# Performance work log

Hardware: AMD Instinct MI355X
Metric: run time of the kernel (lower is better)

Reference implementation:

```python
import jax, jax.numpy as jnp
import numpy as np

B, S, H = 2, 512, 1024
D = 24            # hdim_proj_dim
MLP_H = 96        # hdim_mlp_hidden
VAL_IN = 2 * H    # concat_only
OUT_HID = 2 * max(128, H // 2)  # 1024


def setup_inputs() -> dict:
    key = jax.random.key(0)
    ks = jax.random.split(key, 12)
    sc = 0.02
    return {
        "H_j": jax.random.normal(ks[0], (B, S, H), jnp.float32),
        "H_i": jax.random.normal(ks[1], (B, S, H), jnp.float32),
        "attn_mask": jnp.ones((B, S), jnp.float32),
        "p_j": jax.random.normal(ks[2], (H, D), jnp.float32) * sc,
        "p_i": jax.random.normal(ks[3], (H, D), jnp.float32) * sc,
        "W1": jax.random.normal(ks[4], (4 * D, MLP_H), jnp.float32) * sc,
        "b1": jnp.zeros((MLP_H,), jnp.float32),
        "W2": jax.random.normal(ks[5], (MLP_H, 1), jnp.float32) * sc,
        "b2": jnp.zeros((1,), jnp.float32),
        "Wv1": jax.random.normal(ks[6], (VAL_IN, OUT_HID), jnp.float32) * sc,
        "bv1": jnp.zeros((OUT_HID,), jnp.float32),
        "Wv2": jax.random.normal(ks[7], (OUT_HID, H), jnp.float32) * sc,
        "bv2": jnp.zeros((H,), jnp.float32),
        "alpha": jnp.asarray(0.05, jnp.float32),
    }


def reference(H_j, H_i, attn_mask, p_j, p_i, W1, b1, W2, b2, Wv1, bv1, Wv2, bv2, alpha):
    # Low-dim projections: [B,S,D]
    Zj = jnp.einsum('bsh,hd->bsd', H_j, p_j)
    Zi = jnp.einsum('bsh,hd->bsd', H_i, p_i)
    # 4-term pairwise features: [B,S,S,4D]
    Zj_b = jnp.broadcast_to(Zj[:, :, None, :], (B, S, S, D))
    Zi_b = jnp.broadcast_to(Zi[:, None, :, :], (B, S, S, D))
    pair = jnp.concatenate([Zj_b, Zi_b, Zj_b * Zi_b, jnp.abs(Zj_b - Zi_b)], axis=-1)
    # Pair-score MLP -> logits [B,S,S]
    h = jax.nn.relu(jnp.einsum('bjif,fm->bjim', pair, W1) + b1)
    logits = (jnp.einsum('bjim,mo->bjio', h, W2) + b2)[..., 0]
    # additive key-side mask (same as torch _expand_mask_last)
    logits = logits + (1.0 - attn_mask)[:, None, :] * jnp.finfo(logits.dtype).min
    # token_temp == 1.0 -> no scaling
    probs = jax.nn.softmax(logits, axis=-1)  # over keys i
    ctx = jnp.einsum('bji,bih->bjh', probs, H_i)  # [B,S,H]
    # Value fusion MLP (concat_only), dropout is identity in eval
    msg_in = jnp.concatenate([ctx, H_j], axis=-1)  # [B,S,2H]
    msg = jax.nn.relu(jnp.einsum('bsf,fo->bso', msg_in, Wv1) + bv1)
    msg = jnp.einsum('bso,oh->bsh', msg, Wv2) + bv2
    return alpha * msg
```

## Files before the change

### kernel.cpp

```cpp
#include <hip/hip_runtime.h>
#include <math.h>

#define B_    2
#define S_    512
#define HDIM  1024
#define D_    24
#define M_    96
#define ROWS  (B_*S_)

typedef _Float16 half8 __attribute__((ext_vector_type(8)));
typedef float    f32x4 __attribute__((ext_vector_type(4)));

__device__ __forceinline__ void transpose_tile(
    const float* __restrict__ in, _Float16* __restrict__ out,
    int R, int C, int xt, int yt, float (*tile)[33], int t) {
  int bx = xt * 32, by = yt * 32;
  int tx = t & 31, ty = t >> 5;
#pragma unroll
  for (int k = 0; k < 4; ++k)
    tile[ty + k * 8][tx] = in[(size_t)(by + ty + k * 8) * C + bx + tx];
  __syncthreads();
#pragma unroll
  for (int k = 0; k < 4; ++k)
    out[(size_t)(bx + ty + k * 8) * R + by + tx] = (_Float16)tile[tx][ty + k * 8];
}

__global__ __launch_bounds__(256) void prep_kernel(
    const float* __restrict__ Hj, const float* __restrict__ Hi,
    const float* __restrict__ pj, const float* __restrict__ pi,
    const float* __restrict__ W1, const float* __restrict__ Wv1,
    const float* __restrict__ Wv2,
    _Float16* __restrict__ HjH, _Float16* __restrict__ HiT,
    _Float16* __restrict__ Wv1T, _Float16* __restrict__ Wv2T,
    _Float16* __restrict__ Wimg, float* __restrict__ Zj,
    float* __restrict__ Zi) {
  __shared__ float tile[32][33];
  const int bid = blockIdx.x;
  const int t = threadIdx.x;

  if (bid < 4) {
    int c = bid * 256 + t;
    half8 v = {};
    if (c < 864) {
      int kc = c / 96, m = c - kc * 96;
#pragma unroll
      for (int e = 0; e < 8; ++e)
        v[e] = (_Float16)W1[(24 + kc * 8 + e) * M_ + m];
    }
    *(half8*)(Wimg + (size_t)c * 8) = v;
  } else if (bid < 1028) {
    int i = (bid - 4) * 256 + t;
    float4 v = ((const float4*)Hj)[i];
    _Float16 o[4] = {(_Float16)v.x, (_Float16)v.y, (_Float16)v.z, (_Float16)v.w};
    ((ushort4*)HjH)[i] = *(ushort4*)o;
  } else if (bid < 2052) {
    int id = bid - 1028;
    int z = id >> 9, rem = id & 511;
    transpose_tile(Hi + (size_t)z * S_ * HDIM, HiT + (size_t)z * HDIM * S_,
                   S_, HDIM, rem & 31, rem >> 5, tile, t);
  } else if (bid < 4100) {
    int id = bid - 2052;
    transpose_tile(Wv1, Wv1T, 2 * HDIM, HDIM, id & 31, id >> 5, tile, t);
  } else if (bid < 5124) {
    int id = bid - 4100;
    transpose_tile(Wv2, Wv2T, HDIM, HDIM, id & 31, id >> 5, tile, t);
  } else {
    int r = (bid - 5124) * 4 + (t >> 6);
    int lane = t & 63;
    float4 a4 = ((const float4*)(Hj + (size_t)r * HDIM))[lane];
    float4 c4 = ((const float4*)(Hi + (size_t)r * HDIM))[lane];
    float accj[D_], acci[D_];
#pragma unroll
    for (int d = 0; d < D_; ++d) { accj[d] = 0.f; acci[d] = 0.f; }
    const float* aa = (const float*)&a4;
    const float* cc = (const float*)&c4;
#pragma unroll
    for (int kk = 0; kk < 4; ++kk) {
      const float4* pj4 = (const float4*)(pj + (size_t)(lane * 4 + kk) * D_);
      const float4* pi4 = (const float4*)(pi + (size_t)(lane * 4 + kk) * D_);
      float a = aa[kk], c = cc[kk];
#pragma unroll
      for (int q = 0; q < 6; ++q) {
        float4 wj = pj4[q], wi = pi4[q];
        accj[q * 4 + 0] = fmaf(a, wj.x, accj[q * 4 + 0]);
        accj[q * 4 + 1] = fmaf(a, wj.y, accj[q * 4 + 1]);
        accj[q * 4 + 2] = fmaf(a, wj.z, accj[q * 4 + 2]);
        accj[q * 4 + 3] = fmaf(a, wj.w, accj[q * 4 + 3]);
        acci[q * 4 + 0] = fmaf(c, wi.x, acci[q * 4 + 0]);
        acci[q * 4 + 1] = fmaf(c, wi.y, acci[q * 4 + 1]);
        acci[q * 4 + 2] = fmaf(c, wi.z, acci[q * 4 + 2]);
        acci[q * 4 + 3] = fmaf(c, wi.w, acci[q * 4 + 3]);
      }
    }
#pragma unroll
    for (int d = 0; d < D_; ++d) {
      for (int off = 32; off > 0; off >>= 1) {
        accj[d] += __shfl_down(accj[d], off, 64);
        acci[d] += __shfl_down(acci[d], off, 64);
      }
    }
    if (lane == 0) {
#pragma unroll
      for (int d = 0; d < D_; ++d) {
        Zj[r * D_ + d] = accj[d];
        Zi[r * D_ + d] = acci[d];
      }
    }
  }
}

#define FOFFB   0
#define WOFFB   40960
#define ZOFFB   (WOFFB + 960*16)
#define LOGOFFB (WOFFB + 16384)
#define ZJOFFB  (LOGOFFB + 2048)
#define W2OFFB  (ZJOFFB + 96)
#define REDOFFB (W2OFFB + 384)
#define LDSB    (REDOFFB + 32)

__global__ __launch_bounds__(256) void pair_fused_kernel(
    const float* __restrict__ Zj, const float* __restrict__ Zi,
    const float* __restrict__ W1, const float* __restrict__ b1,
    const float* __restrict__ W2, const _Float16* __restrict__ Wimg,
    const float* __restrict__ mask, _Float16* __restrict__ probs) {
  __shared__ __attribute__((aligned(16))) char smem[LDSB];
  const int t = threadIdx.x;
  const int w = t >> 6, l = t & 63;
  const int lo = l & 15, hi = l >> 4;
  const int rj = blockIdx.x;
  const int b = rj >> 9;

#pragma unroll
  for (int r = 0; r < 4; ++r) {
    const _Float16* src = Wimg + (size_t)(r * 256 + w * 64 + l) * 8;
    __builtin_amdgcn_global_load_lds(
        (const __attribute__((address_space(1))) void*)src,
        (__attribute__((address_space(3))) void*)(smem + WOFFB + (r * 256 + w * 64) * 16),
        16, 0, 0);
  }
  float* zjL    = (float*)(smem + ZJOFFB);
  float* W2s    = (float*)(smem + W2OFFB);
  float* logits = (float*)(smem + LOGOFFB);
  float* red    = (float*)(smem + REDOFFB);
  if (t < D_) zjL[t] = Zj[(size_t)rj * D_ + t];
  if (t < M_) W2s[t] = W2[t];
  float aj = 0.f;
  if (t < M_) {
    aj = b1[t];
#pragma unroll
    for (int d = 0; d < D_; ++d)
      aj = fmaf(Zj[(size_t)rj * D_ + d], W1[d * M_ + t], aj);
  }
  __syncthreads();
  if (t < M_) {
    half8 v = {};
    v[0] = (_Float16)aj;
    *(half8*)(smem + WOFFB + (864 + t) * 16) = v;
  }

  half8 wf[6][3];
  float w2r[6][4];

  for (int p = 0; p < 2; ++p) {
    {
      int i = p * 256 + t;
      const float* zi = Zi + (size_t)(b * S_ + i) * D_;
      float ziv[D_];
#pragma unroll
      for (int q = 0; q < 6; ++q) {
        float4 v = ((const float4*)zi)[q];
        ziv[q * 4 + 0] = v.x; ziv[q * 4 + 1] = v.y;
        ziv[q * 4 + 2] = v.z; ziv[q * 4 + 3] = v.w;
      }
#pragma unroll
      for (int kc = 0; kc < 3; ++kc) {
        half8 v;
#pragma unroll
        for (int e = 0; e < 8; ++e) v[e] = (_Float16)ziv[kc * 8 + e];
        *(half8*)(smem + FOFFB + (kc * 256 + t) * 16) = v;
      }
#pragma unroll
      for (int kc = 0; kc < 3; ++kc) {
        half8 v;
#pragma unroll
        for (int e = 0; e < 8; ++e) {
          int d = kc * 8 + e;
          v[e] = (_Float16)(zjL[d] * ziv[d]);
        }
        *(half8*)(smem + FOFFB + ((kc + 3) * 256 + t) * 16) = v;
      }
#pragma unroll
      for (int kc = 0; kc < 3; ++kc) {
        half8 v;
#pragma unroll
        for (int e = 0; e < 8; ++e) {
          int d = kc * 8 + e;
          v[e] = (_Float16)fabsf(zjL[d] - ziv[d]);
        }
        *(half8*)(smem + FOFFB + ((kc + 6) * 256 + t) * 16) = v;
      }
      if (p == 0) {
        half8 v = {};
        v[0] = (_Float16)1.0f;
        *(half8*)(smem + FOFFB + (9 * 256 + t) * 16) = v;
      }
    }
    __syncthreads();

    if (p == 0) {
#pragma unroll
      for (int mh = 0; mh < 6; ++mh) {
#pragma unroll
        for (int ks = 0; ks < 3; ++ks) {
          int kc = ks * 4 + hi;
          int off = (kc < 10) ? (WOFFB + (kc * 96 + mh * 16 + lo) * 16) : ZOFFB;
          wf[mh][ks] = *(const half8*)(smem + off);
        }
#pragma unroll
        for (int r = 0; r < 4; ++r) w2r[mh][r] = W2s[mh * 16 + hi * 4 + r];
      }
    }

#pragma unroll
    for (int nt = 0; nt < 4; ++nt) {
      half8 ff[3];
#pragma unroll
      for (int ks = 0; ks < 3; ++ks) {
        int kc = ks * 4 + hi;
        int off = (kc < 10) ? (FOFFB + (kc * 256 + w * 64 + nt * 16 + lo) * 16) : ZOFFB;
        ff[ks] = *(const half8*)(smem + off);
      }
      f32x4 a6[6] = {};
#pragma unroll
      for (int ks = 0; ks < 3; ++ks)
#pragma unroll
        for (int mh = 0; mh < 6; ++mh)
          a6[mh] = __builtin_amdgcn_mfma_f32_16x16x32_f16(wf[mh][ks], ff[ks], a6[mh], 0, 0, 0);
      float part = 0.f;
#pragma unroll
      for (int mh = 0; mh < 6; ++mh)
#pragma unroll
        for (int r = 0; r < 4; ++r)
          part = fmaf(fmaxf(a6[mh][r], 0.f), w2r[mh][r], part);
      part += __shfl_xor(part, 16);
      part += __shfl_xor(part, 32);
      if (hi == 0) logits[p * 256 + w * 64 + nt * 16 + lo] = part;
    }
    __syncthreads();
  }

  float m1 = mask[b * S_ + t], m2 = mask[b * S_ + t + 256];
  float lg1 = logits[t]       + (1.0f - m1) * (-3.40282347e38f);
  float lg2 = logits[t + 256] + (1.0f - m2) * (-3.40282347e38f);
  float mx = fmaxf(lg1, lg2);
#pragma unroll
  for (int off = 32; off > 0; off >>= 1) mx = fmaxf(mx, __shfl_xor(mx, off));
  if (l == 0) red[w] = mx;
  __syncthreads();
  float rmax = fmaxf(fmaxf(red[0], red[1]), fmaxf(red[2], red[3]));
  float e1 = __expf(lg1 - rmax);
  float e2 = __expf(lg2 - rmax);
  float s = e1 + e2;
#pragma unroll
  for (int off = 32; off > 0; off >>= 1) s += __shfl_xor(s, off);
  if (l == 0) red[4 + w] = s;
  __syncthreads();
  float inv = 1.0f / (red[4] + red[5] + red[6] + red[7]);
  probs[(size_t)rj * S_ + t]       = (_Float16)(e1 * inv);
  probs[(size_t)rj * S_ + t + 256] = (_Float16)(e2 * inv);
}

template <bool HASA1, bool RELU, bool FINAL, bool OUTH>
__global__ __launch_bounds__(512) void mfma_gemm_kernel(
    const _Float16* __restrict__ A0, const _Float16* __restrict__ A1,
    const _Float16* __restrict__ Bt, const float* __restrict__ bias,
    const float* __restrict__ alpha_ptr, void* __restrict__ Cout,
    int M, int N, int K0, int K1,
    long aB0, long aB1, long bB, long cB) {
  __shared__ __attribute__((aligned(16))) char smem[65536];
  const int t = threadIdx.x;
  const int w = t >> 6, l = t & 63;
  const int g = w >> 2, wq = w & 3;
  const int K = K0 + K1;
  const int KH = K >> 1;
  const int NT = KH >> 5;
  const int n0 = blockIdx.x * 64, m0 = blockIdx.y * 64;
  const int zb = blockIdx.z;
  const _Float16* A0b = A0 + (size_t)zb * aB0;
  const _Float16* A1b = HASA1 ? (A1 + (size_t)zb * aB1) : nullptr;
  const _Float16* Btb = Bt + (size_t)zb * bB;
  char* gls = smem + (g << 15);

  const int sr = (wq << 4) + (l >> 2);
  const int sk = ((l & 3) ^ ((l >> 3) & 3)) << 3;

  const int mq = wq >> 1, nq = wq & 1;
  int offA[2], offB[2];
#pragma unroll
  for (int i = 0; i < 2; ++i) {
    int ra = mq * 32 + i * 16 + (l & 15);
    offA[i] = ra * 64 + (((l >> 4) ^ ((ra >> 1) & 3)) << 4);
    int rb = nq * 32 + i * 16 + (l & 15);
    offB[i] = 4096 + rb * 64 + (((l >> 4) ^ ((rb >> 1) & 3)) << 4);
  }

  f32x4 acc[2][2] = {};

  auto stage = [&](int tt) {
    char* buf = gls + (tt & 3) * 8192;
    int kg = g * KH + (tt << 5) + sk;
    const _Float16* ga;
    if (HASA1 && kg >= K0) ga = A1b + (size_t)(m0 + sr) * K1 + (kg - K0);
    else                   ga = A0b + (size_t)(m0 + sr) * K0 + kg;
    __builtin_amdgcn_global_load_lds(
        (const __attribute__((address_space(1))) void*)ga,
        (__attribute__((address_space(3))) void*)(buf + (wq << 10)), 16, 0, 0);
    const _Float16* gb = Btb + (size_t)(n0 + sr) * K + kg;
    __builtin_amdgcn_global_load_lds(
        (const __attribute__((address_space(1))) void*)gb,
        (__attribute__((address_space(3))) void*)(buf + 4096 + (wq << 10)), 16, 0, 0);
  };

  stage(0);
  stage(1);
  stage(2);

  for (int tt = 0; tt < NT; ++tt) {
    if (tt + 2 < NT)      asm volatile("s_waitcnt vmcnt(4)" ::: "memory");
    else if (tt + 1 < NT) asm volatile("s_waitcnt vmcnt(2)" ::: "memory");
    else                  asm volatile("s_waitcnt vmcnt(0)" ::: "memory");
    __builtin_amdgcn_s_barrier();
    __builtin_amdgcn_sched_barrier(0);
    const char* buf = gls + (tt & 3) * 8192;
    half8 a0 = *(const half8*)(buf + offA[0]);
    half8 a1 = *(const half8*)(buf + offA[1]);
    half8 b0 = *(const half8*)(buf + offB[0]);
    half8 b1v = *(const half8*)(buf + offB[1]);
    acc[0][0] = __builtin_amdgcn_mfma_f32_16x16x32_f16(a0, b0, acc[0][0], 0, 0, 0);
    acc[0][1] = __builtin_amdgcn_mfma_f32_16x16x32_f16(a0, b1v, acc[0][1], 0, 0, 0);
    acc[1][0] = __builtin_amdgcn_mfma_f32_16x16x32_f16(a1, b0, acc[1][0], 0, 0, 0);
    acc[1][1] = __builtin_amdgcn_mfma_f32_16x16x32_f16(a1, b1v, acc[1][1], 0, 0, 0);
    if (tt + 3 < NT) stage(tt + 3);
  }

  const int lr = l & 15, lq = l >> 4;
  float* redm = (float*)smem;
  __syncthreads();
  if (g == 1) {
#pragma unroll
    for (int mi = 0; mi < 2; ++mi)
#pragma unroll
      for (int ni = 0; ni < 2; ++ni)
#pragma unroll
        for (int rg = 0; rg < 4; ++rg)
          redm[(mq * 32 + mi * 16 + lq * 4 + rg) * 68 + nq * 32 + ni * 16 + lr] =
              acc[mi][ni][rg];
  }
  __syncthreads();
  if (g == 0) {
    const float alpha = FINAL ? *alpha_ptr : 1.0f;
    const size_t cbase = (size_t)zb * cB;
#pragma unroll
    for (int mi = 0; mi < 2; ++mi)
#pragma unroll
      for (int ni = 0; ni < 2; ++ni) {
        int col = n0 + nq * 32 + ni * 16 + lr;
        float bv = bias ? bias[col] : 0.0f;
#pragma unroll
        for (int rg = 0; rg < 4; ++rg) {
          int row = m0 + mq * 32 + mi * 16 + lq * 4 + rg;
          float x = acc[mi][ni][rg] +
                    redm[(mq * 32 + mi * 16 + lq * 4 + rg) * 68 + nq * 32 + ni * 16 + lr] +
                    bv;
          if (RELU) x = fmaxf(x, 0.f);
          if (FINAL) x *= alpha;
          if (OUTH)
            ((_Float16*)Cout)[cbase + (size_t)row * N + col] = (_Float16)x;
          else
            ((float*)Cout)[cbase + (size_t)row * N + col] = x;
        }
      }
  }
}

extern "C" void kernel_launch(void* const* d_in, const int* in_sizes, int n_in,
                              void* d_out, int out_size, void* d_ws, size_t ws_size,
                              hipStream_t stream) {
  const float* Hj   = (const float*)d_in[0];
  const float* Hi   = (const float*)d_in[1];
  const float* mask = (const float*)d_in[2];
  const float* pj   = (const float*)d_in[3];
  const float* pi   = (const float*)d_in[4];
  const float* W1   = (const float*)d_in[5];
  const float* b1   = (const float*)d_in[6];
  const float* W2   = (const float*)d_in[7];
  const float* Wv1  = (const float*)d_in[9];
  const float* bv1  = (const float*)d_in[10];
  const float* Wv2  = (const float*)d_in[11];
  const float* bv2  = (const float*)d_in[12];
  const float* alpha = (const float*)d_in[13];

  char* w = (char*)d_ws;
  float* Zj  = (float*)w;            w += (size_t)ROWS * D_ * 4;
  float* Zi  = (float*)w;            w += (size_t)ROWS * D_ * 4;
  _Float16* Wimg   = (_Float16*)w;   w += (size_t)1024 * 16;
  _Float16* probsH = (_Float16*)w;   w += (size_t)B_ * S_ * S_ * 2;
  _Float16* HjH    = (_Float16*)w;   w += (size_t)ROWS * HDIM * 2;
  _Float16* HiT    = (_Float16*)w;   w += (size_t)B_ * HDIM * S_ * 2;
  _Float16* Wv1T   = (_Float16*)w;   w += (size_t)HDIM * 2 * HDIM * 2;
  _Float16* Wv2T   = (_Float16*)w;   w += (size_t)HDIM * HDIM * 2;
  _Float16* ctxH   = (_Float16*)w;   w += (size_t)ROWS * HDIM * 2;
  _Float16* hidH   = (_Float16*)w;   w += (size_t)ROWS * HDIM * 2;
  float* out = (float*)d_out;

  prep_kernel<<<5380, 256, 0, stream>>>(Hj, Hi, pj, pi, W1, Wv1, Wv2,
                                        HjH, HiT, Wv1T, Wv2T, Wimg, Zj, Zi);

  pair_fused_kernel<<<ROWS, 256, 0, stream>>>(Zj, Zi, W1, b1, W2, Wimg,
                                              mask, probsH);

  mfma_gemm_kernel<false, false, false, true><<<dim3(16, 8, 2), 512, 0, stream>>>(
      probsH, nullptr, HiT, nullptr, nullptr, ctxH,
      S_, HDIM, S_, 0, (long)S_ * S_, 0, (long)HDIM * S_, (long)S_ * HDIM);
  mfma_gemm_kernel<true, true, false, true><<<dim3(16, 16, 1), 512, 0, stream>>>(
      ctxH, HjH, Wv1T, bv1, nullptr, hidH,
      ROWS, HDIM, HDIM, HDIM, 0, 0, 0, 0);
  mfma_gemm_kernel<false, false, true, false><<<dim3(16, 16, 1), 512, 0, stream>>>(
      hidH, nullptr, Wv2T, bv2, alpha, out,
      ROWS, HDIM, HDIM, 0, 0, 0, 0, 0);
}
```

Baseline: 76.22 us.

## Use 64x64 transpose tiles, fuse projections into cast, 4-way split-K GEMM

The prep kernel moves to 64x64 transpose tiles that convert to fp16 in LDS and write 16-byte vectors. The Zj/Zi projections are folded into per-row blocks that also do the Hj fp16 cast, which cuts the prep grid. The GEMM kernel goes from 2-way to 4-way split-K inside 1024-thread blocks with 128KB LDS, and the three partial results are reduced through LDS. s_setprio is also placed around the MFMA sections. The larger LDS and thread count may reduce occupancy, and the shorter per-group K loop gives less pipelining depth.

```diff
diff --git a/kernel.cpp b/kernel.cpp
--- a/kernel.cpp
+++ b/kernel.cpp
@@ -10,19 +10,68 @@
 
 typedef _Float16 half8 __attribute__((ext_vector_type(8)));
 typedef float    f32x4 __attribute__((ext_vector_type(4)));
-
-__device__ __forceinline__ void transpose_tile(
+typedef unsigned short ushort8 __attribute__((ext_vector_type(8)));
+
+__device__ __forceinline__ void transpose_tile64(
     const float* __restrict__ in, _Float16* __restrict__ out,
-    int R, int C, int xt, int yt, float (*tile)[33], int t) {
-  int bx = xt * 32, by = yt * 32;
-  int tx = t & 31, ty = t >> 5;
-#pragma unroll
-  for (int k = 0; k < 4; ++k)
-    tile[ty + k * 8][tx] = in[(size_t)(by + ty + k * 8) * C + bx + tx];
-  __syncthreads();
-#pragma unroll
-  for (int k = 0; k < 4; ++k)
-    out[(size_t)(bx + ty + k * 8) * R + by + tx] = (_Float16)tile[tx][ty + k * 8];
+    int R, int C, int xt, int yt, _Float16* tileh, int t) {
+  int R0 = yt * 64, C0 = xt * 64;
+  {
+    int r = t >> 4, c4 = (t & 15) * 4;
+#pragma unroll
+    for (int i = 0; i < 4; ++i) {
+      float4 v = *(const float4*)(in + (size_t)(R0 + r + i * 16) * C + C0 + c4);
+      _Float16 o[4] = {(_Float16)v.x, (_Float16)v.y, (_Float16)v.z, (_Float16)v.w};
+      *(ushort4*)(tileh + (r + i * 16) * 72 + c4) = *(ushort4*)o;
+    }
+  }
+  __syncthreads();
+  {
+    int r0 = (t & 7) * 8;
+#pragma unroll
+    for (int p = 0; p < 2; ++p) {
+      int c = p * 32 + (t >> 3);
+      _Float16 o[8];
+#pragma unroll
+      for (int e = 0; e < 8; ++e) o[e] = tileh[(r0 + e) * 72 + c];
+      *(ushort8*)(out + (size_t)(C0 + c) * R + R0 + r0) = *(ushort8*)o;
+    }
+  }
+}
+
+__device__ __forceinline__ void proj_row(
+    float4 h, const float* __restrict__ P, float* __restrict__ Zrow,
+    float* red4, int t) {
+  float acc[D_];
+#pragma unroll
+  for (int d = 0; d < D_; ++d) acc[d] = 0.f;
+  const float* hh = (const float*)&h;
+#pragma unroll
+  for (int kk = 0; kk < 4; ++kk) {
+    const float4* p4 = (const float4*)(P + (size_t)(t * 4 + kk) * D_);
+    float a = hh[kk];
+#pragma unroll
+    for (int q = 0; q < 6; ++q) {
+      float4 w = p4[q];
+      acc[q * 4 + 0] = fmaf(a, w.x, acc[q * 4 + 0]);
+      acc[q * 4 + 1] = fmaf(a, w.y, acc[q * 4 + 1]);
+      acc[q * 4 + 2] = fmaf(a, w.z, acc[q * 4 + 2]);
+      acc[q * 4 + 3] = fmaf(a, w.w, acc[q * 4 + 3]);
+    }
+  }
+  int w = t >> 6, l = t & 63;
+#pragma unroll
+  for (int d = 0; d < D_; ++d) {
+#pragma unroll
+    for (int off = 32; off > 0; off >>= 1) acc[d] += __shfl_xor(acc[d], off);
+  }
+  if (l == 0) {
+#pragma unroll
+    for (int d = 0; d < D_; ++d) red4[w * D_ + d] = acc[d];
+  }
+  __syncthreads();
+  if (t < D_)
+    Zrow[t] = red4[t] + red4[D_ + t] + red4[2 * D_ + t] + red4[3 * D_ + t];
 }
 
 __global__ __launch_bounds__(256) void prep_kernel(
@@ -34,7 +83,7 @@
     _Float16* __restrict__ Wv1T, _Float16* __restrict__ Wv2T,
     _Float16* __restrict__ Wimg, float* __restrict__ Zj,
     float* __restrict__ Zi) {
-  __shared__ float tile[32][33];
+  __shared__ __attribute__((aligned(16))) _Float16 tileh[64 * 72];
   const int bid = blockIdx.x;
   const int t = threadIdx.x;
 
@@ -49,63 +98,26 @@
     }
     *(half8*)(Wimg + (size_t)c * 8) = v;
   } else if (bid < 1028) {
-    int i = (bid - 4) * 256 + t;
-    float4 v = ((const float4*)Hj)[i];
-    _Float16 o[4] = {(_Float16)v.x, (_Float16)v.y, (_Float16)v.z, (_Float16)v.w};
-    ((ushort4*)HjH)[i] = *(ushort4*)o;
+    int r = bid - 4;
+    float4 h = ((const float4*)(Hj + (size_t)r * HDIM))[t];
+    _Float16 o[4] = {(_Float16)h.x, (_Float16)h.y, (_Float16)h.z, (_Float16)h.w};
+    ((ushort4*)HjH)[(size_t)r * 256 + t] = *(ushort4*)o;
+    proj_row(h, pj, Zj + (size_t)r * D_, (float*)tileh, t);
   } else if (bid < 2052) {
-    int id = bid - 1028;
-    int z = id >> 9, rem = id & 511;
-    transpose_tile(Hi + (size_t)z * S_ * HDIM, HiT + (size_t)z * HDIM * S_,
-                   S_, HDIM, rem & 31, rem >> 5, tile, t);
-  } else if (bid < 4100) {
+    int r = bid - 1028;
+    float4 h = ((const float4*)(Hi + (size_t)r * HDIM))[t];
+    proj_row(h, pi, Zi + (size_t)r * D_, (float*)tileh, t);
+  } else if (bid < 2308) {
     int id = bid - 2052;
-    transpose_tile(Wv1, Wv1T, 2 * HDIM, HDIM, id & 31, id >> 5, tile, t);
-  } else if (bid < 5124) {
-    int id = bid - 4100;
-    transpose_tile(Wv2, Wv2T, HDIM, HDIM, id & 31, id >> 5, tile, t);
+    int z = id >> 7, rem = id & 127;
+    transpose_tile64(Hi + (size_t)z * S_ * HDIM, HiT + (size_t)z * HDIM * S_,
+                     S_, HDIM, rem & 15, rem >> 4, tileh, t);
+  } else if (bid < 2820) {
+    int id = bid - 2308;
+    transpose_tile64(Wv1, Wv1T, 2 * HDIM, HDIM, id & 15, id >> 4, tileh, t);
   } else {
-    int r = (bid - 5124) * 4 + (t >> 6);
-    int lane = t & 63;
-    float4 a4 = ((const float4*)(Hj + (size_t)r * HDIM))[lane];
-    float4 c4 = ((const float4*)(Hi + (size_t)r * HDIM))[lane];
-    float accj[D_], acci[D_];
-#pragma unroll
-    for (int d = 0; d < D_; ++d) { accj[d] = 0.f; acci[d] = 0.f; }
-    const float* aa = (const float*)&a4;
-    const float* cc = (const float*)&c4;
-#pragma unroll
-    for (int kk = 0; kk < 4; ++kk) {
-      const float4* pj4 = (const float4*)(pj + (size_t)(lane * 4 + kk) * D_);
-      const float4* pi4 = (const float4*)(pi + (size_t)(lane * 4 + kk) * D_);
-      float a = aa[kk], c = cc[kk];
-#pragma unroll
-      for (int q = 0; q < 6; ++q) {
-        float4 wj = pj4[q], wi = pi4[q];
-        accj[q * 4 + 0] = fmaf(a, wj.x, accj[q * 4 + 0]);
-        accj[q * 4 + 1] = fmaf(a, wj.y, accj[q * 4 + 1]);
-        accj[q * 4 + 2] = fmaf(a, wj.z, accj[q * 4 + 2]);
-        accj[q * 4 + 3] = fmaf(a, wj.w, accj[q * 4 + 3]);
-        acci[q * 4 + 0] = fmaf(c, wi.x, acci[q * 4 + 0]);
-        acci[q * 4 + 1] = fmaf(c, wi.y, acci[q * 4 + 1]);
-        acci[q * 4 + 2] = fmaf(c, wi.z, acci[q * 4 + 2]);
-        acci[q * 4 + 3] = fmaf(c, wi.w, acci[q * 4 + 3]);
-      }
-    }
-#pragma unroll
-    for (int d = 0; d < D_; ++d) {
-      for (int off = 32; off > 0; off >>= 1) {
-        accj[d] += __shfl_down(accj[d], off, 64);
-        acci[d] += __shfl_down(acci[d], off, 64);
-      }
-    }
-    if (lane == 0) {
-#pragma unroll
-      for (int d = 0; d < D_; ++d) {
-        Zj[r * D_ + d] = accj[d];
-        Zi[r * D_ + d] = acci[d];
-      }
-    }
+    int id = bid - 2820;
+    transpose_tile64(Wv2, Wv2T, HDIM, HDIM, id & 15, id >> 4, tileh, t);
   }
 }
 
@@ -231,11 +243,13 @@
         ff[ks] = *(const half8*)(smem + off);
       }
       f32x4 a6[6] = {};
+      __builtin_amdgcn_s_setprio(1);
 #pragma unroll
       for (int ks = 0; ks < 3; ++ks)
 #pragma unroll
         for (int mh = 0; mh < 6; ++mh)
           a6[mh] = __builtin_amdgcn_mfma_f32_16x16x32_f16(wf[mh][ks], ff[ks], a6[mh], 0, 0, 0);
+      __builtin_amdgcn_s_setprio(0);
       float part = 0.f;
 #pragma unroll
       for (int mh = 0; mh < 6; ++mh)
@@ -271,19 +285,19 @@
 }
 
 template <bool HASA1, bool RELU, bool FINAL, bool OUTH>
-__global__ __launch_bounds__(512) void mfma_gemm_kernel(
+__global__ __launch_bounds__(1024) void mfma_gemm_kernel(
     const _Float16* __restrict__ A0, const _Float16* __restrict__ A1,
     const _Float16* __restrict__ Bt, const float* __restrict__ bias,
     const float* __restrict__ alpha_ptr, void* __restrict__ Cout,
     int M, int N, int K0, int K1,
     long aB0, long aB1, long bB, long cB) {
-  __shared__ __attribute__((aligned(16))) char smem[65536];
+  __shared__ __attribute__((aligned(16))) char smem[131072];
   const int t = threadIdx.x;
   const int w = t >> 6, l = t & 63;
   const int g = w >> 2, wq = w & 3;
   const int K = K0 + K1;
-  const int KH = K >> 1;
-  const int NT = KH >> 5;
+  const int KQ = K >> 2;
+  const int NT = KQ >> 5;
   const int n0 = blockIdx.x * 64, m0 = blockIdx.y * 64;
   const int zb = blockIdx.z;
   const _Float16* A0b = A0 + (size_t)zb * aB0;
@@ -308,7 +322,7 @@
 
   auto stage = [&](int tt) {
     char* buf = gls + (tt & 3) * 8192;
-    int kg = g * KH + (tt << 5) + sk;
+    int kg = g * KQ + (tt << 5) + sk;
     const _Float16* ga;
     if (HASA1 && kg >= K0) ga = A1b + (size_t)(m0 + sr) * K1 + (kg - K0);
     else                   ga = A0b + (size_t)(m0 + sr) * K0 + kg;
@@ -322,8 +336,8 @@
   };
 
   stage(0);
-  stage(1);
-  stage(2);
+  if (NT > 1) stage(1);
+  if (NT > 2) stage(2);
 
   for (int tt = 0; tt < NT; ++tt) {
     if (tt + 2 < NT)      asm volatile("s_waitcnt vmcnt(4)" ::: "memory");
@@ -336,24 +350,27 @@
     half8 a1 = *(const half8*)(buf + offA[1]);
     half8 b0 = *(const half8*)(buf + offB[0]);
     half8 b1v = *(const half8*)(buf + offB[1]);
+    __builtin_amdgcn_s_setprio(1);
     acc[0][0] = __builtin_amdgcn_mfma_f32_16x16x32_f16(a0, b0, acc[0][0], 0, 0, 0);
     acc[0][1] = __builtin_amdgcn_mfma_f32_16x16x32_f16(a0, b1v, acc[0][1], 0, 0, 0);
     acc[1][0] = __builtin_amdgcn_mfma_f32_16x16x32_f16(a1, b0, acc[1][0], 0, 0, 0);
     acc[1][1] = __builtin_amdgcn_mfma_f32_16x16x32_f16(a1, b1v, acc[1][1], 0, 0, 0);
+    __builtin_amdgcn_s_setprio(0);
     if (tt + 3 < NT) stage(tt + 3);
   }
 
   const int lr = l & 15, lq = l >> 4;
   float* redm = (float*)smem;
   __syncthreads();
-  if (g == 1) {
+  if (g > 0) {
+    float* rb = redm + (g - 1) * 64 * 68;
 #pragma unroll
     for (int mi = 0; mi < 2; ++mi)
 #pragma unroll
       for (int ni = 0; ni < 2; ++ni)
 #pragma unroll
         for (int rg = 0; rg < 4; ++rg)
-          redm[(mq * 32 + mi * 16 + lq * 4 + rg) * 68 + nq * 32 + ni * 16 + lr] =
+          rb[(mq * 32 + mi * 16 + lq * 4 + rg) * 68 + nq * 32 + ni * 16 + lr] =
               acc[mi][ni][rg];
   }
   __syncthreads();
@@ -369,9 +386,9 @@
 #pragma unroll
         for (int rg = 0; rg < 4; ++rg) {
           int row = m0 + mq * 32 + mi * 16 + lq * 4 + rg;
-          float x = acc[mi][ni][rg] +
-                    redm[(mq * 32 + mi * 16 + lq * 4 + rg) * 68 + nq * 32 + ni * 16 + lr] +
-                    bv;
+          int ri = (mq * 32 + mi * 16 + lq * 4 + rg) * 68 + nq * 32 + ni * 16 + lr;
+          float x = acc[mi][ni][rg] + redm[ri] + redm[64 * 68 + ri] +
+                    redm[2 * 64 * 68 + ri] + bv;
           if (RELU) x = fmaxf(x, 0.f);
           if (FINAL) x *= alpha;
           if (OUTH)
@@ -413,19 +430,19 @@
   _Float16* hidH   = (_Float16*)w;   w += (size_t)ROWS * HDIM * 2;
   float* out = (float*)d_out;
 
-  prep_kernel<<<5380, 256, 0, stream>>>(Hj, Hi, pj, pi, W1, Wv1, Wv2,
+  prep_kernel<<<3076, 256, 0, stream>>>(Hj, Hi, pj, pi, W1, Wv1, Wv2,
                                         HjH, HiT, Wv1T, Wv2T, Wimg, Zj, Zi);
 
   pair_fused_kernel<<<ROWS, 256, 0, stream>>>(Zj, Zi, W1, b1, W2, Wimg,
                                               mask, probsH);
 
-  mfma_gemm_kernel<false, false, false, true><<<dim3(16, 8, 2), 512, 0, stream>>>(
+  mfma_gemm_kernel<false, false, false, true><<<dim3(16, 8, 2), 1024, 0, stream>>>(
       probsH, nullptr, HiT, nullptr, nullptr, ctxH,
       S_, HDIM, S_, 0, (long)S_ * S_, 0, (long)HDIM * S_, (long)S_ * HDIM);
-  mfma_gemm_kernel<true, true, false, true><<<dim3(16, 16, 1), 512, 0, stream>>>(
+  mfma_gemm_kernel<true, true, false, true><<<dim3(16, 16, 1), 1024, 0, stream>>>(
       ctxH, HjH, Wv1T, bv1, nullptr, hidH,
       ROWS, HDIM, HDIM, HDIM, 0, 0, 0, 0);
-  mfma_gemm_kernel<false, false, true, false><<<dim3(16, 16, 1), 512, 0, stream>>>(
+  mfma_gemm_kernel<false, false, true, false><<<dim3(16, 16, 1), 1024, 0, stream>>>(
       hidH, nullptr, Wv2T, bv2, alpha, out,
       ROWS, HDIM, HDIM, 0, 0, 0, 0, 0);
 }
```

New measurement: 84.77 us. 11.2% more time.
